# Kernel optimization log

Measured on AMD Instinct MI355X. Metric: run time of the kernel, lower is better.

Reference implementation:

```python
import jax, jax.numpy as jnp
import numpy as np

N_NODES = 50000
N_EDGES = 800000
N_GRAPHS = 512
IN_F = 128
HEADS = 8
HEAD_C = 8
OUT_F = HEADS * HEAD_C  # 64
NEG_SLOPE = 0.2


def setup_inputs() -> dict:
    key = jax.random.key(0)
    ks = jax.random.split(key, 10)
    x = jax.random.normal(ks[0], (N_NODES, IN_F), dtype=jnp.float32)
    edge_index = jax.random.randint(ks[1], (2, N_EDGES), 0, N_NODES, dtype=jnp.int64)
    batch = jnp.sort(jax.random.randint(ks[2], (N_NODES,), 0, N_GRAPHS, dtype=jnp.int64))
    s = 0.05
    W = jax.random.normal(ks[3], (IN_F, OUT_F), dtype=jnp.float32) * s
    att_src = jax.random.normal(ks[4], (HEADS, HEAD_C), dtype=jnp.float32) * s
    att_dst = jax.random.normal(ks[5], (HEADS, HEAD_C), dtype=jnp.float32) * s
    bias = jax.random.normal(ks[6], (OUT_F,), dtype=jnp.float32) * s
    pool_w_rel = jax.random.normal(ks[7], (OUT_F, 1), dtype=jnp.float32) * s
    pool_b_rel = jax.random.normal(ks[8], (1,), dtype=jnp.float32) * s
    pool_w_root = jax.random.normal(ks[9], (OUT_F, 1), dtype=jnp.float32) * s
    return {"x": x, "edge_index": edge_index, "batch": batch, "W": W,
            "att_src": att_src, "att_dst": att_dst, "bias": bias,
            "pool_w_rel": pool_w_rel, "pool_b_rel": pool_b_rel,
            "pool_w_root": pool_w_root}


def _segment_softmax(e, seg, num_segments):
    # numerically stable scatter-softmax over segments
    m = jax.ops.segment_max(e, seg, num_segments=num_segments)
    ex = jnp.exp(e - m[seg])
    denom = jax.ops.segment_sum(ex, seg, num_segments=num_segments)
    return ex / (denom[seg] + 1e-16)


def reference(x, edge_index, batch, W, att_src, att_dst, bias,
              pool_w_rel, pool_b_rel, pool_w_root):
    N = N_NODES
    # ---- GATConv (concat heads, self-loops added, LeakyReLU 0.2) ----
    loops = jnp.arange(N, dtype=edge_index.dtype)
    src = jnp.concatenate([edge_index[0], loops])
    dst = jnp.concatenate([edge_index[1], loops])
    h = (x @ W).reshape(N, HEADS, HEAD_C)                 # [N,H,C]
    a_s = jnp.einsum('nhc,hc->nh', h, att_src)            # [N,H]
    a_d = jnp.einsum('nhc,hc->nh', h, att_dst)
    e = jax.nn.leaky_relu(a_s[src] + a_d[dst], NEG_SLOPE) # [E+N,H]
    alpha = _segment_softmax(e, dst, N)                   # softmax over incoming edges
    out = jax.ops.segment_sum(h[src] * alpha[:, :, None], dst, num_segments=N)
    out = out.reshape(N, OUT_F) + bias                    # [N,64]
    # ---- SAGPooling(min_score=-1): GraphConv score + per-graph softmax,
    #      all nodes kept (softmax scores > -1), features scaled by score ----
    s2, d2 = edge_index[0], edge_index[1]
    aggr = jax.ops.segment_sum(out[s2], d2, num_segments=N)  # add-aggregation
    score = (aggr @ pool_w_rel + pool_b_rel + out @ pool_w_root)[:, 0]  # [N]
    score = _segment_softmax(score, batch, N_GRAPHS)
    att_x = out * score[:, None]
    # ---- global_add_pool ----
    g = jax.ops.segment_sum(att_x, batch, num_segments=N_GRAPHS)  # [G,64]
    return out, g
```

## Files before the change

kernel.cpp:

```cpp
#include <hip/hip_runtime.h>

#define NN 50000
#define NE 800000
#define NG 512
#define INF_ 128
#define OUTF 64
#define CAP 64

#define NPB 98
#define BSHIFT 9
#define BNODES 512
#define BCAP 9216
#define NCHUNK 250
#define BCH 3200

#define GEMM_BLOCKS ((NN + 63) / 64)
#define FRONT_BLOCKS 1032

#define XSTRIDE 136

__device__ __forceinline__ unsigned short f2bf(float f) {
    unsigned int u = __float_as_uint(f);
    unsigned int r = (u + 0x7fffu + ((u >> 16) & 1u)) >> 16;
    return (unsigned short)r;
}
__device__ __forceinline__ float bf2f(unsigned int lo16) {
    return __uint_as_float(lo16 << 16);
}

using bf16x8 = __attribute__((ext_vector_type(8))) __bf16;
using f32x4  = __attribute__((ext_vector_type(4))) float;

__global__ __launch_bounds__(256) void k_front(
    const int* __restrict__ ei, int* __restrict__ bcnt,
    unsigned int* __restrict__ ebuf, float* __restrict__ gden,
    float* __restrict__ g_num,
    const float* __restrict__ x, const float* __restrict__ W,
    const float* __restrict__ att_src, const float* __restrict__ att_dst,
    unsigned short* __restrict__ hb, float* __restrict__ a_s,
    float* __restrict__ a_d)
{
    __shared__ union {
        struct {
            unsigned short Wt[OUTF * XSTRIDE];
            unsigned short Xs[64 * XSTRIDE];
        } g;
        struct {
            int hist[128];
            int bofs[128];
            int goff[128];
            unsigned int pk[BCH];
            unsigned int ord[BCH];
        } b;
    } sm;

    {
        int idx = blockIdx.x * 256 + threadIdx.x;
        if (idx < NG) gden[idx] = 0.f;
        else if (idx < NG + NG * OUTF) g_num[idx - NG] = 0.f;
    }

    const int t = threadIdx.x;
    int gemmIdx;
    if (blockIdx.x < 1000) {
        const int oct = blockIdx.x >> 2;
        const int r   = blockIdx.x & 3;
        if (r == 0) {
            if (t < 128) sm.b.hist[t] = 0;
            __syncthreads();

            const int e0 = oct * BCH;
            for (int i = t; i < BCH; i += 256) {
                int e = e0 + i;
                int s = ei[e];
                int d = ei[NE + e];
                int bb = d >> BSHIFT;
                unsigned int v = ((unsigned int)bb << 25) |
                                 ((unsigned int)(d & (BNODES - 1)) << 16) |
                                 (unsigned int)s;
                sm.b.pk[i] = v;
                atomicAdd(&sm.b.hist[bb], 1);
            }
            __syncthreads();

            if (t < 64) {
                int c0 = sm.b.hist[2 * t];
                int c1 = sm.b.hist[2 * t + 1];
                int p  = c0 + c1;
                int ip = p;
                #pragma unroll
                for (int m = 1; m < 64; m <<= 1) {
                    int o = __shfl_up(ip, m, 64);
                    if (t >= m) ip += o;
                }
                int epair = ip - p;
                int ex0 = epair;
                int ex1 = epair + c0;
                int g0 = (2 * t     < NPB) ? atomicAdd(&bcnt[2 * t],     c0) : 0;
                int g1 = (2 * t + 1 < NPB) ? atomicAdd(&bcnt[2 * t + 1], c1) : 0;
                sm.b.bofs[2 * t]     = ex0;
                sm.b.bofs[2 * t + 1] = ex1;
                sm.b.goff[2 * t]     = g0;
                sm.b.goff[2 * t + 1] = g1;
                sm.b.hist[2 * t]     = ex0;
                sm.b.hist[2 * t + 1] = ex1;
            }
            __syncthreads();

            for (int i = t; i < BCH; i += 256) {
                unsigned int v = sm.b.pk[i];
                int bb = v >> 25;
                int p = atomicAdd(&sm.b.hist[bb], 1);
                sm.b.ord[p] = v;
            }
            __syncthreads();

            for (int i = t; i < BCH; i += 256) {
                unsigned int v = sm.b.ord[i];
                int bb = v >> 25;
                int gp = sm.b.goff[bb] + (i - sm.b.bofs[bb]);
                if (gp < BCAP) ebuf[(size_t)bb * BCAP + gp] = v;
            }
            return;
        }
        gemmIdx = oct * 3 + (r - 1);
    } else {
        gemmIdx = 750 + (blockIdx.x - 1000);
    }

    const int n0 = gemmIdx * 64;

    #pragma unroll
    for (int it = 0; it < 8; it++) {
        int i = it * 256 + t;
        int k  = i >> 4;
        int n4 = (i & 15) * 4;
        float4 v = ((const float4*)W)[i];
        sm.g.Wt[(n4 + 0) * XSTRIDE + k] = f2bf(v.x);
        sm.g.Wt[(n4 + 1) * XSTRIDE + k] = f2bf(v.y);
        sm.g.Wt[(n4 + 2) * XSTRIDE + k] = f2bf(v.z);
        sm.g.Wt[(n4 + 3) * XSTRIDE + k] = f2bf(v.w);
    }

    #pragma unroll
    for (int it = 0; it < 8; it++) {
        int idx = it * 256 + t;
        int row = idx >> 5;
        int c4  = idx & 31;
        int n = n0 + row;
        if (n > NN - 1) n = NN - 1;
        float4 v = ((const float4*)(x + (size_t)n * INF_))[c4];
        ushort4 b;
        b.x = f2bf(v.x); b.y = f2bf(v.y); b.z = f2bf(v.z); b.w = f2bf(v.w);
        *(ushort4*)&sm.g.Xs[row * XSTRIDE + c4 * 4] = b;
    }
    __syncthreads();

    const int lane = t & 63;
    const int w    = t >> 6;
    const int q    = lane & 15;
    const int h4   = lane >> 4;

    f32x4 acc[4];
    #pragma unroll
    for (int ct = 0; ct < 4; ct++) acc[ct] = (f32x4){0.f, 0.f, 0.f, 0.f};

    const unsigned short* Ax = &sm.g.Xs[(w * 16 + q) * XSTRIDE + h4 * 8];
    const unsigned short* Bw = &sm.g.Wt[q * XSTRIDE + h4 * 8];

    #pragma unroll
    for (int ks = 0; ks < 4; ks++) {
        bf16x8 av = *(const bf16x8*)(Ax + ks * 32);
        #pragma unroll
        for (int ct = 0; ct < 4; ct++) {
            bf16x8 bv = *(const bf16x8*)(Bw + ct * 16 * XSTRIDE + ks * 32);
            acc[ct] = __builtin_amdgcn_mfma_f32_16x16x32_bf16(av, bv, acc[ct], 0, 0, 0);
        }
    }

    float atts[4], attd[4];
    #pragma unroll
    for (int ct = 0; ct < 4; ct++) {
        int head = 2 * ct + (q >> 3);
        atts[ct] = att_src[head * 8 + (q & 7)];
        attd[ct] = att_dst[head * 8 + (q & 7)];
    }

    #pragma unroll
    for (int r = 0; r < 4; r++) {
        const int n = n0 + w * 16 + h4 * 4 + r;
        const bool valid = (n < NN);
        if (valid) {
            #pragma unroll
            for (int ct = 0; ct < 4; ct++)
                hb[(size_t)n * OUTF + ct * 16 + q] = f2bf(acc[ct][r]);
        }
        float ps[4], pd[4];
        #pragma unroll
        for (int ct = 0; ct < 4; ct++) {
            float v = acc[ct][r];
            ps[ct] = v * atts[ct];
            pd[ct] = v * attd[ct];
        }
        #pragma unroll
        for (int m = 1; m < 8; m <<= 1) {
            #pragma unroll
            for (int ct = 0; ct < 4; ct++) {
                ps[ct] += __shfl_xor(ps[ct], m, 64);
                pd[ct] += __shfl_xor(pd[ct], m, 64);
            }
        }
        if (valid && (q & 7) == 0) {
            #pragma unroll
            for (int ct = 0; ct < 4; ct++) {
                int head = 2 * ct + (q >> 3);
                a_s[n * 8 + head] = ps[ct];
                a_d[n * 8 + head] = pd[ct];
            }
        }
    }
}

#define BHALF 256
__global__ __launch_bounds__(256) void k_build(
    const unsigned int* __restrict__ ebuf, const int* __restrict__ bcnt,
    int* __restrict__ deg, unsigned short* __restrict__ adj)
{
    __shared__ unsigned short ladj[BHALF * CAP];
    __shared__ int ldeg[BHALF];

    const int b    = blockIdx.x >> 1;
    const int half = blockIdx.x & 1;
    const int rlo  = half * BHALF;
    const int t    = threadIdx.x;

    if (t < BHALF) ldeg[t] = 0;
    __syncthreads();

    const int cnt = min(bcnt[b], BCAP);
    const unsigned int* eb = ebuf + (size_t)b * BCAP;
    for (int i = t; i < cnt; i += 256) {
        unsigned int v = eb[i];
        int drel = (v >> 16) & (BNODES - 1);
        unsigned int rr = (unsigned int)(drel - rlo);
        if (rr < BHALF) {
            int p = atomicAdd(&ldeg[rr], 1);
            if (p < CAP) ladj[rr * CAP + p] = (unsigned short)(v & 0xffffu);
        }
    }
    __syncthreads();

    const int n0 = b * BNODES + rlo;
    if (t < BHALF) {
        int n = n0 + t;
        if (n < NN) deg[n] = ldeg[t];
    }
    for (int i = t; i < BHALF * CAP / 8; i += 256) {
        int n = n0 + (i >> 3);
        if (n < NN)
            ((uint4*)(adj + (size_t)n * CAP))[i & 7] = ((const uint4*)ladj)[i];
    }
}

__global__ __launch_bounds__(256) void k_aggr(
    const unsigned short* __restrict__ hb, const float* __restrict__ a_s,
    const float* __restrict__ a_d, const int* __restrict__ deg,
    const unsigned short* __restrict__ adj, const float* __restrict__ bias,
    const float* __restrict__ w_rel, const float* __restrict__ w_root,
    float* __restrict__ out, float* __restrict__ t_rel, float* __restrict__ t_root)
{
    const int wid  = threadIdx.x >> 6;
    const int lane = threadIdx.x & 63;
    const int g    = lane >> 3;
    const int c8   = lane & 7;
    const int n    = blockIdx.x * 4 + wid;
    if (n >= NN) return;

    const float ad_n = a_d[n * 8 + c8];

    float acc[8];
    #pragma unroll
    for (int k = 0; k < 8; k++) acc[k] = 0.f;
    float den = 0.f;

    if (g == 0) {
        float e0 = a_s[n * 8 + c8] + ad_n;
        e0 = e0 > 0.f ? e0 : 0.2f * e0;
        float ex0 = __expf(e0);
        uint4 hv = *(const uint4*)(hb + (size_t)n * OUTF + c8 * 8);
        acc[0] = ex0 * bf2f(hv.x & 0xffffu); acc[1] = ex0 * bf2f(hv.x >> 16);
        acc[2] = ex0 * bf2f(hv.y & 0xffffu); acc[3] = ex0 * bf2f(hv.y >> 16);
        acc[4] = ex0 * bf2f(hv.z & 0xffffu); acc[5] = ex0 * bf2f(hv.z >> 16);
        acc[6] = ex0 * bf2f(hv.w & 0xffffu); acc[7] = ex0 * bf2f(hv.w >> 16);
        den = ex0;
    }

    const int cnt = min(deg[n], CAP);
    const unsigned short* lst = adj + (size_t)n * CAP;

    int sv[4];
    #pragma unroll
    for (int ii = 0; ii < 4; ii++) {
        int i = g + ii * 8;
        sv[ii] = (i < cnt) ? (int)lst[i] : -1;
    }
    float asl[4]; uint4 hvl[4];
    #pragma unroll
    for (int ii = 0; ii < 4; ii++) {
        int s = (sv[ii] >= 0) ? sv[ii] : n;
        asl[ii] = a_s[s * 8 + c8];
        hvl[ii] = *(const uint4*)(hb + (size_t)s * OUTF + c8 * 8);
    }
    #pragma unroll
    for (int ii = 0; ii < 4; ii++) {
        float e = asl[ii] + ad_n;
        e = e > 0.f ? e : 0.2f * e;
        float ex = (sv[ii] >= 0) ? __expf(e) : 0.f;
        uint4 hv = hvl[ii];
        acc[0] = fmaf(ex, bf2f(hv.x & 0xffffu), acc[0]);
        acc[1] = fmaf(ex, bf2f(hv.x >> 16),     acc[1]);
        acc[2] = fmaf(ex, bf2f(hv.y & 0xffffu), acc[2]);
        acc[3] = fmaf(ex, bf2f(hv.y >> 16),     acc[3]);
        acc[4] = fmaf(ex, bf2f(hv.z & 0xffffu), acc[4]);
        acc[5] = fmaf(ex, bf2f(hv.z >> 16),     acc[5]);
        acc[6] = fmaf(ex, bf2f(hv.w & 0xffffu), acc[6]);
        acc[7] = fmaf(ex, bf2f(hv.w >> 16),     acc[7]);
        den += ex;
    }
    for (int i = g + 32; i < cnt; i += 8) {
        int s = lst[i];
        float as = a_s[s * 8 + c8];
        uint4 hv = *(const uint4*)(hb + (size_t)s * OUTF + c8 * 8);
        float e = as + ad_n;
        e = e > 0.f ? e : 0.2f * e;
        float ex = __expf(e);
        acc[0] = fmaf(ex, bf2f(hv.x & 0xffffu), acc[0]);
        acc[1] = fmaf(ex, bf2f(hv.x >> 16),     acc[1]);
        acc[2] = fmaf(ex, bf2f(hv.y & 0xffffu), acc[2]);
        acc[3] = fmaf(ex, bf2f(hv.y >> 16),     acc[3]);
        acc[4] = fmaf(ex, bf2f(hv.z & 0xffffu), acc[4]);
        acc[5] = fmaf(ex, bf2f(hv.z >> 16),     acc[5]);
        acc[6] = fmaf(ex, bf2f(hv.w & 0xffffu), acc[6]);
        acc[7] = fmaf(ex, bf2f(hv.w >> 16),     acc[7]);
        den += ex;
    }

    #pragma unroll
    for (int m = 8; m < 64; m <<= 1) {
        den += __shfl_xor(den, m, 64);
        #pragma unroll
        for (int k = 0; k < 8; k++) acc[k] += __shfl_xor(acc[k], m, 64);
    }

    const float inv = 1.f / (den + 1e-16f);
    float o[8];
    #pragma unroll
    for (int k = 0; k < 8; k++) o[k] = acc[k] * inv + bias[c8 * 8 + k];

    if (g == 0) {
        float4 o0 = make_float4(o[0], o[1], o[2], o[3]);
        float4 o1 = make_float4(o[4], o[5], o[6], o[7]);
        float4* op = (float4*)(out + (size_t)n * OUTF + c8 * 8);
        op[0] = o0; op[1] = o1;
    }

    float vr = 0.f, vt = 0.f;
    #pragma unroll
    for (int k = 0; k < 8; k++) {
        vr = fmaf(o[k], w_rel[c8 * 8 + k], vr);
        vt = fmaf(o[k], w_root[c8 * 8 + k], vt);
    }
    #pragma unroll
    for (int m = 1; m < 8; m <<= 1) {
        vr += __shfl_xor(vr, m, 64);
        vt += __shfl_xor(vt, m, 64);
    }
    if (lane == 0) { t_rel[n] = vr; t_root[n] = vt; }
}

__global__ __launch_bounds__(256) void k_score_pool(
    const int* __restrict__ deg, const unsigned short* __restrict__ adj,
    const float* __restrict__ t_rel, const float* __restrict__ t_root,
    const float* __restrict__ pool_b, const int* __restrict__ batch,
    const float* __restrict__ out,
    float* __restrict__ gden, float* __restrict__ g_num)
{
    __shared__ float ex_s[32];
    __shared__ int   b_s[32];

    const int wid  = threadIdx.x >> 6;
    const int lane = threadIdx.x & 63;
    const int sub  = lane >> 3;
    const int g    = lane & 7;
    const int base_n = blockIdx.x * 32;
    const int n    = base_n + wid * 8 + sub;

    const int cnt = (n < NN) ? min(deg[n], CAP) : 0;
    const unsigned short* lst = adj + (size_t)n * CAP;
    float acc = 0.f;
    for (int i = g; i < cnt; i += 8) acc += t_rel[lst[i]];
    #pragma unroll
    for (int m = 1; m < 8; m <<= 1) acc += __shfl_xor(acc, m, 64);

    if (g == 0) {
        const int slot = wid * 8 + sub;
        if (n < NN) {
            float ex = __expf(acc + t_root[n] + pool_b[0]);
            ex_s[slot] = ex;
            b_s[slot]  = batch[n];
        } else {
            ex_s[slot] = 0.f;
            b_s[slot]  = -1;
        }
    }
    __syncthreads();

    if (threadIdx.x == 0) {
        float racc = 0.f;
        int bcur = -1;
        for (int i = 0; i < 32; i++) {
            int b = b_s[i];
            if (b != bcur) {
                if (bcur >= 0) atomicAdd(&gden[bcur], racc);
                bcur = b; racc = 0.f;
            }
            racc += ex_s[i];
        }
        if (bcur >= 0) atomicAdd(&gden[bcur], racc);
    }

    const int j = lane;
    float facc = 0.f;
    int bcur = -1;
    for (int i = 0; i < 8; i++) {
        const int slot = wid * 8 + i;
        const int n2 = base_n + slot;
        if (n2 >= NN) break;
        int b = b_s[slot];
        if (b != bcur) {
            if (bcur >= 0) atomicAdd(&g_num[bcur * OUTF + j], facc);
            bcur = b; facc = 0.f;
        }
        facc = fmaf(out[(size_t)n2 * OUTF + j], ex_s[slot], facc);
    }
    if (bcur >= 0) atomicAdd(&g_num[bcur * OUTF + j], facc);
}

__global__ __launch_bounds__(256) void k_gfinal(
    const float* __restrict__ g_num, const float* __restrict__ gden,
    float* __restrict__ g)
{
    int i = blockIdx.x * 256 + threadIdx.x;
    if (i < NG * OUTF) g[i] = g_num[i] / (gden[i >> 6] + 1e-16f);
}

extern "C" void kernel_launch(void* const* d_in, const int* in_sizes, int n_in,
                              void* d_out, int out_size, void* d_ws, size_t ws_size,
                              hipStream_t stream)
{
    const float* x        = (const float*)d_in[0];
    const int*   ei       = (const int*)  d_in[1];
    const int*   batch    = (const int*)  d_in[2];
    const float* W        = (const float*)d_in[3];
    const float* att_src  = (const float*)d_in[4];
    const float* att_dst  = (const float*)d_in[5];
    const float* bias     = (const float*)d_in[6];
    const float* w_rel    = (const float*)d_in[7];
    const float* pool_b   = (const float*)d_in[8];
    const float* w_root   = (const float*)d_in[9];

    float* out_nodes = (float*)d_out;
    float* g_out     = (float*)d_out + (size_t)NN * OUTF;

    char* base = (char*)d_ws;
    unsigned short* hb = (unsigned short*)(base);
    float* a_s       = (float*)(base +  6400000);
    float* a_d       = (float*)(base +  8000000);
    float* t_rel     = (float*)(base +  9600000);
    float* t_root    = (float*)(base +  9800000);
    float* gden      = (float*)(base + 10000000);
    float* g_num     = (float*)(base + 10002048);
    int*   deg       = (int*)  (base + 10133120);
    unsigned short* adjl = (unsigned short*)(base + 10333120);
    unsigned int* ebuf = (unsigned int*)(base + 16733120);
    int*   bcnt      = (int*)  (base + 20345792);

    hipMemsetAsync(bcnt, 0, 512, stream);

    k_front<<<FRONT_BLOCKS, 256, 0, stream>>>(
        ei, bcnt, ebuf, gden, g_num,
        x, W, att_src, att_dst, hb, a_s, a_d);
    k_build<<<NPB * 2, 256, 0, stream>>>(ebuf, bcnt, deg, adjl);
    k_aggr<<<(NN + 3) / 4, 256, 0, stream>>>(hb, a_s, a_d, deg, adjl, bias,
                                             w_rel, w_root, out_nodes, t_rel, t_root);
    k_score_pool<<<(NN + 31) / 32, 256, 0, stream>>>(deg, adjl, t_rel, t_root,
                                                     pool_b, batch, out_nodes,
                                                     gden, g_num);
    k_gfinal<<<(NG * OUTF + 255) / 256, 256, 0, stream>>>(g_num, gden, g_out);
}
```

Measured before the change: 166.9 us.

## Double GEMM rows per block and batch score gather loads

The front kernel's GEMM tile grows from 64 to 128 rows per block. Each wave now computes two 16-row MFMA tiles that share the same W operand loads, and the block mix is rebalanced to one bucketing block per GEMM block, cutting total blocks from 1032 to 641. The score kernel's neighbour gather now issues its first four t_rel loads unconditionally in an unrolled batch to expose memory-level parallelism, with a loop handling the tail. The cost is more shared memory and registers per block, which may lower occupancy.

Result: no change. 164.7 us (-1.3%).

```diff
diff --git a/kernel.cpp b/kernel.cpp
--- a/kernel.cpp
+++ b/kernel.cpp
@@ -14,8 +14,8 @@
 #define NCHUNK 250
 #define BCH 3200
 
-#define GEMM_BLOCKS ((NN + 63) / 64)
-#define FRONT_BLOCKS 1032
+#define GEMM2_BLOCKS ((NN + 127) / 128)
+#define FRONT_BLOCKS 641
 
 #define XSTRIDE 136
 
@@ -43,7 +43,7 @@
     __shared__ union {
         struct {
             unsigned short Wt[OUTF * XSTRIDE];
-            unsigned short Xs[64 * XSTRIDE];
+            unsigned short Xs[128 * XSTRIDE];
         } g;
         struct {
             int hist[128];
@@ -62,14 +62,13 @@
 
     const int t = threadIdx.x;
     int gemmIdx;
-    if (blockIdx.x < 1000) {
-        const int oct = blockIdx.x >> 2;
-        const int r   = blockIdx.x & 3;
-        if (r == 0) {
+    if (blockIdx.x < 500) {
+        const int pr = blockIdx.x >> 1;
+        if ((blockIdx.x & 1) == 0) {
             if (t < 128) sm.b.hist[t] = 0;
             __syncthreads();
 
-            const int e0 = oct * BCH;
+            const int e0 = pr * BCH;
             for (int i = t; i < BCH; i += 256) {
                 int e = e0 + i;
                 int s = ei[e];
@@ -123,12 +122,12 @@
             }
             return;
         }
-        gemmIdx = oct * 3 + (r - 1);
+        gemmIdx = pr;
     } else {
-        gemmIdx = 750 + (blockIdx.x - 1000);
-    }
-
-    const int n0 = gemmIdx * 64;
+        gemmIdx = 250 + (blockIdx.x - 500);
+    }
+
+    const int n0 = gemmIdx * 128;
 
     #pragma unroll
     for (int it = 0; it < 8; it++) {
@@ -143,7 +142,7 @@
     }
 
     #pragma unroll
-    for (int it = 0; it < 8; it++) {
+    for (int it = 0; it < 16; it++) {
         int idx = it * 256 + t;
         int row = idx >> 5;
         int c4  = idx & 31;
@@ -161,20 +160,25 @@
     const int q    = lane & 15;
     const int h4   = lane >> 4;
 
-    f32x4 acc[4];
-    #pragma unroll
-    for (int ct = 0; ct < 4; ct++) acc[ct] = (f32x4){0.f, 0.f, 0.f, 0.f};
-
-    const unsigned short* Ax = &sm.g.Xs[(w * 16 + q) * XSTRIDE + h4 * 8];
-    const unsigned short* Bw = &sm.g.Wt[q * XSTRIDE + h4 * 8];
+    f32x4 acc[2][4];
+    #pragma unroll
+    for (int rt = 0; rt < 2; rt++)
+        #pragma unroll
+        for (int ct = 0; ct < 4; ct++) acc[rt][ct] = (f32x4){0.f, 0.f, 0.f, 0.f};
+
+    const unsigned short* Ax0 = &sm.g.Xs[(w * 32 + q) * XSTRIDE + h4 * 8];
+    const unsigned short* Ax1 = &sm.g.Xs[(w * 32 + 16 + q) * XSTRIDE + h4 * 8];
+    const unsigned short* Bw  = &sm.g.Wt[q * XSTRIDE + h4 * 8];
 
     #pragma unroll
     for (int ks = 0; ks < 4; ks++) {
-        bf16x8 av = *(const bf16x8*)(Ax + ks * 32);
+        bf16x8 a0 = *(const bf16x8*)(Ax0 + ks * 32);
+        bf16x8 a1 = *(const bf16x8*)(Ax1 + ks * 32);
         #pragma unroll
         for (int ct = 0; ct < 4; ct++) {
             bf16x8 bv = *(const bf16x8*)(Bw + ct * 16 * XSTRIDE + ks * 32);
-            acc[ct] = __builtin_amdgcn_mfma_f32_16x16x32_bf16(av, bv, acc[ct], 0, 0, 0);
+            acc[0][ct] = __builtin_amdgcn_mfma_f32_16x16x32_bf16(a0, bv, acc[0][ct], 0, 0, 0);
+            acc[1][ct] = __builtin_amdgcn_mfma_f32_16x16x32_bf16(a1, bv, acc[1][ct], 0, 0, 0);
         }
     }
 
@@ -187,35 +191,38 @@
     }
 
     #pragma unroll
-    for (int r = 0; r < 4; r++) {
-        const int n = n0 + w * 16 + h4 * 4 + r;
-        const bool valid = (n < NN);
-        if (valid) {
-            #pragma unroll
-            for (int ct = 0; ct < 4; ct++)
-                hb[(size_t)n * OUTF + ct * 16 + q] = f2bf(acc[ct][r]);
-        }
-        float ps[4], pd[4];
+    for (int rt = 0; rt < 2; rt++) {
         #pragma unroll
-        for (int ct = 0; ct < 4; ct++) {
-            float v = acc[ct][r];
-            ps[ct] = v * atts[ct];
-            pd[ct] = v * attd[ct];
-        }
-        #pragma unroll
-        for (int m = 1; m < 8; m <<= 1) {
+        for (int r = 0; r < 4; r++) {
+            const int n = n0 + w * 32 + rt * 16 + h4 * 4 + r;
+            const bool valid = (n < NN);
+            if (valid) {
+                #pragma unroll
+                for (int ct = 0; ct < 4; ct++)
+                    hb[(size_t)n * OUTF + ct * 16 + q] = f2bf(acc[rt][ct][r]);
+            }
+            float ps[4], pd[4];
             #pragma unroll
             for (int ct = 0; ct < 4; ct++) {
-                ps[ct] += __shfl_xor(ps[ct], m, 64);
-                pd[ct] += __shfl_xor(pd[ct], m, 64);
-            }
-        }
-        if (valid && (q & 7) == 0) {
+                float v = acc[rt][ct][r];
+                ps[ct] = v * atts[ct];
+                pd[ct] = v * attd[ct];
+            }
             #pragma unroll
-            for (int ct = 0; ct < 4; ct++) {
-                int head = 2 * ct + (q >> 3);
-                a_s[n * 8 + head] = ps[ct];
-                a_d[n * 8 + head] = pd[ct];
+            for (int m = 1; m < 8; m <<= 1) {
+                #pragma unroll
+                for (int ct = 0; ct < 4; ct++) {
+                    ps[ct] += __shfl_xor(ps[ct], m, 64);
+                    pd[ct] += __shfl_xor(pd[ct], m, 64);
+                }
+            }
+            if (valid && (q & 7) == 0) {
+                #pragma unroll
+                for (int ct = 0; ct < 4; ct++) {
+                    int head = 2 * ct + (q >> 3);
+                    a_s[n * 8 + head] = ps[ct];
+                    a_d[n * 8 + head] = pd[ct];
+                }
             }
         }
     }
@@ -397,8 +404,24 @@
 
     const int cnt = (n < NN) ? min(deg[n], CAP) : 0;
     const unsigned short* lst = adj + (size_t)n * CAP;
+
+    int sv[4];
+    #pragma unroll
+    for (int ii = 0; ii < 4; ii++) {
+        int i = g + ii * 8;
+        sv[ii] = (i < cnt) ? (int)lst[i] : -1;
+    }
+    float tv[4];
+    #pragma unroll
+    for (int ii = 0; ii < 4; ii++) {
+        int s = (sv[ii] >= 0) ? sv[ii] : 0;
+        tv[ii] = t_rel[s];
+    }
     float acc = 0.f;
-    for (int i = g; i < cnt; i += 8) acc += t_rel[lst[i]];
+    #pragma unroll
+    for (int ii = 0; ii < 4; ii++)
+        acc += (sv[ii] >= 0) ? tv[ii] : 0.f;
+    for (int i = g + 32; i < cnt; i += 8) acc += t_rel[lst[i]];
     #pragma unroll
     for (int m = 1; m < 8; m <<= 1) acc += __shfl_xor(acc, m, 64);
 
```
